# Optimization experiments

Hardware: AMD Instinct MI355X
Metric: run time of the kernel (lower is better)

Reference implementation:

```python
import jax, jax.numpy as jnp
import numpy as np

D_MODEL = 1024
NUM_HEADS = 16
D_K = D_MODEL // NUM_HEADS
ROPE_THETA = 10000.0


def setup_inputs() -> dict:
    key = jax.random.key(0)
    kx, kq, kk, kv, ko = jax.random.split(key, 5)
    B, S = 2, 2048
    sigma = np.sqrt(2.0) / np.sqrt(D_MODEL + D_MODEL)
    x = jax.random.normal(kx, (B, S, D_MODEL), dtype=jnp.float32)
    Wq = jax.random.normal(kq, (D_MODEL, D_MODEL), dtype=jnp.float32) * sigma
    Wk = jax.random.normal(kk, (D_MODEL, D_MODEL), dtype=jnp.float32) * sigma
    Wv = jax.random.normal(kv, (D_MODEL, D_MODEL), dtype=jnp.float32) * sigma
    Wo = jax.random.normal(ko, (D_MODEL, D_MODEL), dtype=jnp.float32) * sigma
    return {"x": x, "Wq": Wq, "Wk": Wk, "Wv": Wv, "Wo": Wo}


def _rope(t, positions):
    # t: [B, H, S, D_K], positions: [S]
    half = jnp.arange(0, D_K, 2, dtype=jnp.float32)          # [D_K/2]
    freqs = 1.0 / (ROPE_THETA ** (half / D_K))               # [D_K/2]
    angles = positions[:, None].astype(jnp.float32) * freqs  # [S, D_K/2]
    cos = jnp.cos(angles)
    sin = jnp.sin(angles)
    t_even = t[..., 0::2]
    t_odd = t[..., 1::2]
    even_rot = t_even * cos - t_odd * sin
    odd_rot = t_even * sin + t_odd * cos
    # interleave back to [..., D_K]
    return jnp.stack([even_rot, odd_rot], axis=-1).reshape(t.shape)


def reference(x, Wq, Wk, Wv, Wo):
    B, S, _ = x.shape
    # weight layout is [d_out, d_in]: y = x @ W.T
    def proj(W):
        y = jnp.einsum('bsd,ed->bse', x, W)
        return y.reshape(B, S, NUM_HEADS, D_K).transpose(0, 2, 1, 3)  # [B,H,S,Dk]
    Q, K, V = proj(Wq), proj(Wk), proj(Wv)
    positions = jnp.arange(S)
    Q = _rope(Q, positions)
    K = _rope(K, positions)
    scale = 1.0 / jnp.sqrt(jnp.asarray(D_K, dtype=x.dtype))
    scores = jnp.einsum('bhqd,bhkd->bhqk', Q, K) * scale  # [B,H,S,S]
    causal = jnp.tril(jnp.ones((S, S), dtype=bool))
    scores = jnp.where(causal, scores, -jnp.inf)
    probs = jax.nn.softmax(scores, axis=-1)
    out = jnp.einsum('bhqk,bhkd->bhqd', probs, V)          # [B,H,S,Dk]
    out = out.transpose(0, 2, 1, 3).reshape(B, S, D_MODEL)
    return jnp.einsum('bsd,ed->bse', out, Wo)
```

## Files before the change

### kernel.cpp

```cpp
#include <hip/hip_runtime.h>
#include <hip/hip_bf16.h>
#include <math.h>

#define S_LEN   2048
#define BATCH   2
#define DMODEL  1024
#define NHEADS  16
#define DKH     64
#define MROWS   (BATCH * S_LEN)

typedef __attribute__((ext_vector_type(8))) __bf16 bf16x8;
typedef __attribute__((ext_vector_type(4))) float f32x4;
typedef __attribute__((ext_vector_type(8))) unsigned short u16x8;

__device__ __forceinline__ float bfu2f(unsigned short u) {
    union { unsigned int i; float f; } v;
    v.i = ((unsigned int)u) << 16;
    return v.f;
}

__device__ __forceinline__ unsigned short f2bfu(float f) {
    union { __bf16 h; unsigned short u; } v;
    v.h = (__bf16)f;
    return v.u;
}

#define LGKM0() __builtin_amdgcn_s_waitcnt(0xc07f)

#define VMCNT_BAR(n) do {                                        \
    asm volatile("s_waitcnt vmcnt(" #n ")" ::: "memory");        \
    __builtin_amdgcn_s_barrier();                                \
    __builtin_amdgcn_sched_barrier(0);                           \
} while (0)

__device__ __forceinline__ void gload_lds16(const void* g, void* l) {
    __builtin_amdgcn_global_load_lds(
        (const __attribute__((address_space(1))) void*)g,
        (__attribute__((address_space(3))) void*)l, 16, 0, 0);
}

__global__ __launch_bounds__(256) void cvt_all(
    const float* __restrict__ W0, const float* __restrict__ W1, const float* __restrict__ W2,
    const float* __restrict__ X,
    unsigned short* __restrict__ Wb,
    unsigned short* __restrict__ Xb)
{
    const int y = blockIdx.y;
    const float* src;
    unsigned short* dst;
    if (y < 3) {
        src = (y == 0) ? W0 : (y == 1) ? W1 : W2;
        dst = Wb + (size_t)y * (DMODEL * DMODEL);
    } else {
        src = X + (size_t)(y - 3) * (DMODEL * DMODEL);
        dst = Xb + (size_t)(y - 3) * (DMODEL * DMODEL);
    }
    size_t idx = ((size_t)blockIdx.x * 256 + threadIdx.x) * 8;
    float4 a = *(const float4*)(src + idx);
    float4 b = *(const float4*)(src + idx + 4);
    u16x8 h;
    h[0] = f2bfu(a.x); h[1] = f2bfu(a.y); h[2] = f2bfu(a.z); h[3] = f2bfu(a.w);
    h[4] = f2bfu(b.x); h[5] = f2bfu(b.y); h[6] = f2bfu(b.z); h[7] = f2bfu(b.w);
    *(u16x8*)(dst + idx) = h;
}

__global__ __launch_bounds__(256) void cvt_wo(
    const float* __restrict__ W, unsigned short* __restrict__ Wob)
{
    size_t idx = ((size_t)blockIdx.x * 256 + threadIdx.x) * 8;
    float4 a = *(const float4*)(W + idx);
    float4 b = *(const float4*)(W + idx + 4);
    u16x8 h;
    h[0] = f2bfu(a.x); h[1] = f2bfu(a.y); h[2] = f2bfu(a.z); h[3] = f2bfu(a.w);
    h[4] = f2bfu(b.x); h[5] = f2bfu(b.y); h[6] = f2bfu(b.z); h[7] = f2bfu(b.w);
    *(u16x8*)(Wob + idx) = h;
}

__global__ __launch_bounds__(256) void gemm_qkv(
    const unsigned short* __restrict__ Xb,
    const unsigned short* __restrict__ Wb,
    unsigned short* __restrict__ Yq, unsigned short* __restrict__ Yk, unsigned short* __restrict__ Yv)
{
    __shared__ __align__(16) unsigned char pool[49152];
    unsigned short* base = (unsigned short*)pool;

    const int tid  = threadIdx.x;
    const int wave = tid >> 6;
    const int lane = tid & 63;
    const int c    = lane & 15;
    const int quad = lane >> 4;

    const int m0 = blockIdx.y * 128;
    const int n0 = blockIdx.x * 128;
    const int w_idx = n0 >> 10;
    const int e0    = n0 & 1023;
    const unsigned short* Wsrc = Wb + (size_t)w_idx * (DMODEL * DMODEL);

    const int mhalf = (wave & 1) * 64;
    const int nhalf = (wave >> 1) * 64;

    f32x4 acc[4][4];
#pragma unroll
    for (int i = 0; i < 4; i++)
#pragma unroll
        for (int j = 0; j < 4; j++) acc[i][j] = (f32x4){0.f, 0.f, 0.f, 0.f};

    const int srow = wave * 32 + (lane >> 2);
    const int scol = (lane & 3) * 8;
    const unsigned short* Asrc = Xb   + (size_t)(m0 + srow) * DMODEL + scol;
    const unsigned short* Bsrc = Wsrc + (size_t)(e0 + srow) * DMODEL + scol;
    const int doff = srow * 32 + scol;

#define QKV_STAGE(buf, kt) do {                                                    \
    unsigned short* _A = base + (buf) * 8192;                                      \
    unsigned short* _B = _A + 4096;                                                \
    const int _k0 = (kt) * 32;                                                     \
    _Pragma("unroll")                                                              \
    for (int _j = 0; _j < 2; _j++) {                                               \
        gload_lds16(Asrc + (size_t)(_j * 16) * DMODEL + _k0, _A + doff + _j * 512);\
        gload_lds16(Bsrc + (size_t)(_j * 16) * DMODEL + _k0, _B + doff + _j * 512);\
    }                                                                              \
} while (0)

#define QKV_COMPUTE(buf) do {                                                      \
    const unsigned short* _A = base + (buf) * 8192;                                \
    const unsigned short* _B = _A + 4096;                                          \
    bf16x8 af[4], bfr[4];                                                          \
    _Pragma("unroll")                                                              \
    for (int mt = 0; mt < 4; mt++)                                                 \
        af[mt] = *(const bf16x8*)(&_A[(mhalf + mt * 16 + c) * 32 + quad * 8]);     \
    _Pragma("unroll")                                                              \
    for (int nt = 0; nt < 4; nt++)                                                 \
        bfr[nt] = *(const bf16x8*)(&_B[(nhalf + nt * 16 + c) * 32 + quad * 8]);    \
    _Pragma("unroll")                                                              \
    for (int mt = 0; mt < 4; mt++)                                                 \
        _Pragma("unroll")                                                          \
        for (int nt = 0; nt < 4; nt++)                                             \
            acc[mt][nt] = __builtin_amdgcn_mfma_f32_16x16x32_bf16(af[mt], bfr[nt], acc[mt][nt], 0, 0, 0); \
} while (0)

    QKV_STAGE(0, 0);
    QKV_STAGE(1, 1);
    for (int g = 0; g < 10; ++g) {
        const int t = g * 3;
        VMCNT_BAR(4); QKV_STAGE(2, t + 2); QKV_COMPUTE(0);
        VMCNT_BAR(4); QKV_STAGE(0, t + 3); QKV_COMPUTE(1);
        VMCNT_BAR(4); QKV_STAGE(1, t + 4); QKV_COMPUTE(2);
    }
    VMCNT_BAR(4); QKV_COMPUTE(0);
    VMCNT_BAR(0); QKV_COMPUTE(1);

    __syncthreads();

    const int h = (e0 + nhalf) >> 6;
    if (w_idx < 2) {
        unsigned short* Yqk = (w_idx == 0) ? Yq : Yk;
        float* EPf = (float*)pool + wave * 16 * 68;
        const int row = lane >> 2;
        const int cg  = lane & 3;
#pragma unroll
        for (int mt = 0; mt < 4; mt++) {
            LGKM0();
#pragma unroll
            for (int nt = 0; nt < 4; nt++)
#pragma unroll
                for (int r = 0; r < 4; r++)
                    EPf[(quad * 4 + r) * 68 + nt * 16 + c] = acc[mt][nt][r];
            LGKM0();
            float fl[16];
#pragma unroll
            for (int j = 0; j < 4; j++) {
                float4 v = *(const float4*)(&EPf[row * 68 + cg * 16 + j * 4]);
                fl[j * 4 + 0] = v.x; fl[j * 4 + 1] = v.y;
                fl[j * 4 + 2] = v.z; fl[j * 4 + 3] = v.w;
            }
            int m = m0 + mhalf + mt * 16 + row;
            int s = m & (S_LEN - 1);
            int b = m >> 11;
            u16x8 o0, o1;
#pragma unroll
            for (int pi = 0; pi < 8; pi++) {
                int p = cg * 8 + pi;
                float freq  = exp2f(-(float)p * 0.41524101186092034f);
                float angle = (float)s * freq;
                float sn, cs;
                __sincosf(angle, &sn, &cs);
                float ev = fl[2 * pi], ov = fl[2 * pi + 1];
                float re = ev * cs - ov * sn;
                float ro = ev * sn + ov * cs;
                if (pi < 4) { o0[2 * pi] = f2bfu(re); o0[2 * pi + 1] = f2bfu(ro); }
                else        { o1[2 * (pi - 4)] = f2bfu(re); o1[2 * (pi - 4) + 1] = f2bfu(ro); }
            }
            unsigned short* dst = Yqk + (((size_t)(b * NHEADS + h)) * S_LEN + s) * DKH + cg * 16;
            *(u16x8*)(dst)     = o0;
            *(u16x8*)(dst + 8) = o1;
        }
    } else {
        unsigned short* EPb = (unsigned short*)pool + wave * 64 * 72;
        LGKM0();
#pragma unroll
        for (int nt = 0; nt < 4; nt++)
#pragma unroll
            for (int mt = 0; mt < 4; mt++)
#pragma unroll
                for (int r = 0; r < 4; r++)
                    EPb[(nt * 16 + c) * 72 + mt * 16 + quad * 4 + r] = f2bfu(acc[mt][nt][r]);
        LGKM0();
        int mbase = m0 + mhalf;
        int s0 = mbase & (S_LEN - 1);
        int b  = mbase >> 11;
        unsigned short* dst = Yv + (((size_t)(b * NHEADS + h)) * DKH + lane) * S_LEN + s0;
#pragma unroll
        for (int j = 0; j < 8; j++)
            *(u16x8*)(dst + j * 8) = *(const u16x8*)(&EPb[lane * 72 + j * 8]);
    }
#undef QKV_STAGE
#undef QKV_COMPUTE
}

__global__ __launch_bounds__(256) void gemm_wo(
    const unsigned short* __restrict__ X,
    const unsigned short* __restrict__ Wob,
    float* __restrict__ Yf)
{
    __shared__ __align__(16) unsigned char pool[36864];
    unsigned short* base = (unsigned short*)pool;

    const int tid  = threadIdx.x;
    const int wave = tid >> 6;
    const int lane = tid & 63;
    const int c    = lane & 15;
    const int quad = lane >> 4;

    const int m0 = blockIdx.y * 64;
    const int n0 = blockIdx.x * 128;

    const int mhalf = (wave & 1) * 32;
    const int nhalf = (wave >> 1) * 64;

    f32x4 acc[2][4];
#pragma unroll
    for (int i = 0; i < 2; i++)
#pragma unroll
        for (int j = 0; j < 4; j++) acc[i][j] = (f32x4){0.f, 0.f, 0.f, 0.f};

    const int arow = wave * 16 + (lane >> 2);
    const int brow = wave * 32 + (lane >> 2);
    const int scol = (lane & 3) * 8;
    const unsigned short* Asrc = X   + (size_t)(m0 + arow) * DMODEL + scol;
    const unsigned short* Bsrc = Wob + (size_t)(n0 + brow) * DMODEL + scol;
    const int adoff = arow * 32 + scol;
    const int bdoff = brow * 32 + scol;

#define WO_STAGE(buf, kt) do {                                                     \
    unsigned short* _A = base + (buf) * 6144;                                      \
    unsigned short* _B = _A + 2048;                                                \
    const int _k0 = (kt) * 32;                                                     \
    gload_lds16(Asrc + _k0, _A + adoff);                                           \
    _Pragma("unroll")                                                              \
    for (int _j = 0; _j < 2; _j++)                                                 \
        gload_lds16(Bsrc + (size_t)(_j * 16) * DMODEL + _k0, _B + bdoff + _j * 512);\
} while (0)

#define WO_COMPUTE(buf) do {                                                       \
    const unsigned short* _A = base + (buf) * 6144;                                \
    const unsigned short* _B = _A + 2048;                                          \
    bf16x8 af[2], bfr[4];                                                          \
    _Pragma("unroll")                                                              \
    for (int mt = 0; mt < 2; mt++)                                                 \
        af[mt] = *(const bf16x8*)(&_A[(mhalf + mt * 16 + c) * 32 + quad * 8]);     \
    _Pragma("unroll")                                                              \
    for (int nt = 0; nt < 4; nt++)                                                 \
        bfr[nt] = *(const bf16x8*)(&_B[(nhalf + nt * 16 + c) * 32 + quad * 8]);    \
    _Pragma("unroll")                                                              \
    for (int mt = 0; mt < 2; mt++)                                                 \
        _Pragma("unroll")                                                          \
        for (int nt = 0; nt < 4; nt++)                                             \
            acc[mt][nt] = __builtin_amdgcn_mfma_f32_16x16x32_bf16(af[mt], bfr[nt], acc[mt][nt], 0, 0, 0); \
} while (0)

    WO_STAGE(0, 0);
    WO_STAGE(1, 1);
    for (int g = 0; g < 10; ++g) {
        const int t = g * 3;
        VMCNT_BAR(3); WO_STAGE(2, t + 2); WO_COMPUTE(0);
        VMCNT_BAR(3); WO_STAGE(0, t + 3); WO_COMPUTE(1);
        VMCNT_BAR(3); WO_STAGE(1, t + 4); WO_COMPUTE(2);
    }
    VMCNT_BAR(3); WO_COMPUTE(0);
    VMCNT_BAR(0); WO_COMPUTE(1);

    __syncthreads();

    float* EPf = (float*)pool + wave * 16 * 68;
    const int row = lane >> 2;
    const int cg  = lane & 3;
#pragma unroll
    for (int mt = 0; mt < 2; mt++) {
        LGKM0();
#pragma unroll
        for (int nt = 0; nt < 4; nt++)
#pragma unroll
            for (int r = 0; r < 4; r++)
                EPf[(quad * 4 + r) * 68 + nt * 16 + c] = acc[mt][nt][r];
        LGKM0();
        int m = m0 + mhalf + mt * 16 + row;
        float* dst = Yf + (size_t)m * DMODEL + n0 + nhalf + cg * 16;
#pragma unroll
        for (int j = 0; j < 4; j++)
            *(float4*)(dst + j * 4) = *(const float4*)(&EPf[row * 68 + cg * 16 + j * 4]);
    }
#undef WO_STAGE
#undef WO_COMPUTE
}

__global__ __launch_bounds__(256, 4) void attn_mfma(
    const unsigned short* __restrict__ Q,
    const unsigned short* __restrict__ K,
    const unsigned short* __restrict__ Vt,
    unsigned short* __restrict__ A)
{
    __shared__ unsigned short Ks[2][32 * 72];
    __shared__ unsigned short Vs[2][64 * 40];
    __shared__ unsigned short Plds[4][16 * 40];

    const int tid  = threadIdx.x;
    const int wave = tid >> 6;
    const int lane = tid & 63;
    const int c    = lane & 15;
    const int quad = lane >> 4;

    const int bh = blockIdx.x;
    const int b  = bh >> 4;
    const int h  = bh & 15;
    const int qb = (int)(gridDim.y - 1) - (int)blockIdx.y;
    const int q0b = qb * 64;
    const int q0 = q0b + wave * 16;

    const unsigned short* Qb = Q  + (size_t)bh * S_LEN * DKH;
    const unsigned short* Kb = K  + (size_t)bh * S_LEN * DKH;
    const unsigned short* Vb = Vt + (size_t)bh * DKH * S_LEN;

    bf16x8 qf0 = *(const bf16x8*)(Qb + (q0 + c) * DKH + quad * 8);
    bf16x8 qf1 = *(const bf16x8*)(Qb + (q0 + c) * DKH + 32 + quad * 8);

    f32x4 o0 = {0.f,0.f,0.f,0.f}, o1 = o0, o2 = o0, o3 = o0;
    float l[4] = {0.f, 0.f, 0.f, 0.f};

    unsigned short* Pw = &Plds[wave][0];

    const int my_nkb   = (q0 + 16 + 31) >> 5;
    const int nkb_blk  = (q0b + 64 + 31) >> 5;
    const int kb_full  = (q0 >= 31) ? (((q0 - 31) >> 5) + 1) : 0;

    const int krow  = tid >> 3;
    const int kcol8 = (tid & 7) * 8;
    const int vrow  = tid >> 2;
    const int vcol8 = (tid & 3) * 8;

    uint4 gK = *(const uint4*)(Kb + (size_t)krow * DKH + kcol8);
    uint4 gV = *(const uint4*)(Vb + (size_t)vrow * S_LEN + vcol8);
    *(uint4*)(&Ks[0][krow * 72 + kcol8]) = gK;
    *(uint4*)(&Vs[0][vrow * 40 + vcol8]) = gV;

    for (int kb = 0; kb < nkb_blk; kb++) {
        const int k0 = kb * 32;
        const int nb = kb + 1;
        const bool pre = nb < nkb_blk;
        __syncthreads();
        if (pre) {
            gK = *(const uint4*)(Kb + (size_t)(nb * 32 + krow) * DKH + kcol8);
            gV = *(const uint4*)(Vb + (size_t)vrow * S_LEN + nb * 32 + vcol8);
        }
        if (kb < my_nkb) {
            const unsigned short* Kc = &Ks[kb & 1][0];
            const unsigned short* Vc = &Vs[kb & 1][0];
            bf16x8 k00 = *(const bf16x8*)(&Kc[c * 72 + quad * 8]);
            bf16x8 k01 = *(const bf16x8*)(&Kc[c * 72 + 32 + quad * 8]);
            bf16x8 k10 = *(const bf16x8*)(&Kc[(16 + c) * 72 + quad * 8]);
            bf16x8 k11 = *(const bf16x8*)(&Kc[(16 + c) * 72 + 32 + quad * 8]);
            f32x4 s0 = {0.f,0.f,0.f,0.f}, s1 = {0.f,0.f,0.f,0.f};
            __builtin_amdgcn_s_setprio(1);
            s0 = __builtin_amdgcn_mfma_f32_16x16x32_bf16(qf0, k00, s0, 0, 0, 0);
            s0 = __builtin_amdgcn_mfma_f32_16x16x32_bf16(qf1, k01, s0, 0, 0, 0);
            s1 = __builtin_amdgcn_mfma_f32_16x16x32_bf16(qf0, k10, s1, 0, 0, 0);
            s1 = __builtin_amdgcn_mfma_f32_16x16x32_bf16(qf1, k11, s1, 0, 0, 0);
            __builtin_amdgcn_s_setprio(0);

            if (kb < kb_full) {
#pragma unroll
                for (int r = 0; r < 4; r++) {
                    float e0 = __expf(s0[r] * 0.125f);
                    float e1 = __expf(s1[r] * 0.125f);
                    unsigned short pb0 = f2bfu(e0);
                    unsigned short pb1 = f2bfu(e1);
                    Pw[(quad * 4 + r) * 40 + c]      = pb0;
                    Pw[(quad * 4 + r) * 40 + 16 + c] = pb1;
                    l[r] += bfu2f(pb0) + bfu2f(pb1);
                }
            } else {
#pragma unroll
                for (int r = 0; r < 4; r++) {
                    int qrow = q0 + quad * 4 + r;
                    float e0 = (k0 + c      <= qrow) ? __expf(s0[r] * 0.125f) : 0.0f;
                    float e1 = (k0 + 16 + c <= qrow) ? __expf(s1[r] * 0.125f) : 0.0f;
                    unsigned short pb0 = f2bfu(e0);
                    unsigned short pb1 = f2bfu(e1);
                    Pw[(quad * 4 + r) * 40 + c]      = pb0;
                    Pw[(quad * 4 + r) * 40 + 16 + c] = pb1;
                    l[r] += bfu2f(pb0) + bfu2f(pb1);
                }
            }
            LGKM0();

            bf16x8 pf = *(const bf16x8*)(Pw + c * 40 + quad * 8);

            bf16x8 vf0 = *(const bf16x8*)(&Vc[(0 * 16 + c) * 40 + quad * 8]);
            bf16x8 vf1 = *(const bf16x8*)(&Vc[(1 * 16 + c) * 40 + quad * 8]);
            bf16x8 vf2 = *(const bf16x8*)(&Vc[(2 * 16 + c) * 40 + quad * 8]);
            bf16x8 vf3 = *(const bf16x8*)(&Vc[(3 * 16 + c) * 40 + quad * 8]);
            __builtin_amdgcn_s_setprio(1);
            o0 = __builtin_amdgcn_mfma_f32_16x16x32_bf16(pf, vf0, o0, 0, 0, 0);
            o1 = __builtin_amdgcn_mfma_f32_16x16x32_bf16(pf, vf1, o1, 0, 0, 0);
            o2 = __builtin_amdgcn_mfma_f32_16x16x32_bf16(pf, vf2, o2, 0, 0, 0);
            o3 = __builtin_amdgcn_mfma_f32_16x16x32_bf16(pf, vf3, o3, 0, 0, 0);
            __builtin_amdgcn_s_setprio(0);
        }
        if (pre) {
            *(uint4*)(&Ks[nb & 1][krow * 72 + kcol8]) = gK;
            *(uint4*)(&Vs[nb & 1][vrow * 40 + vcol8]) = gV;
        }
    }

#pragma unroll
    for (int m = 1; m < 16; m <<= 1) {
#pragma unroll
        for (int r = 0; r < 4; r++) l[r] += __shfl_xor(l[r], m, 64);
    }

#pragma unroll
    for (int r = 0; r < 4; r++) {
        float inv = 1.0f / l[r];
        int s = q0 + quad * 4 + r;
        unsigned short* Ap = A + ((size_t)b * S_LEN + s) * DMODEL + h * DKH;
        Ap[0 * 16 + c] = f2bfu(o0[r] * inv);
        Ap[1 * 16 + c] = f2bfu(o1[r] * inv);
        Ap[2 * 16 + c] = f2bfu(o2[r] * inv);
        Ap[3 * 16 + c] = f2bfu(o3[r] * inv);
    }
}

extern "C" void kernel_launch(void* const* d_in, const int* in_sizes, int n_in,
                              void* d_out, int out_size, void* d_ws, size_t ws_size,
                              hipStream_t stream) {
    const float* x  = (const float*)d_in[0];
    const float* Wq = (const float*)d_in[1];
    const float* Wk = (const float*)d_in[2];
    const float* Wv = (const float*)d_in[3];
    const float* Wo = (const float*)d_in[4];
    float* out = (float*)d_out;

    unsigned short* Qw = (unsigned short*)d_ws;
    unsigned short* Kw = Qw + (size_t)MROWS * DMODEL;
    unsigned short* Vw = Kw + (size_t)MROWS * DMODEL;
    unsigned short* Wb = Vw + (size_t)MROWS * DMODEL;
    unsigned short* Aw = Wb;
    unsigned short* Wob = Qw;
    unsigned short* Xb = (unsigned short*)d_out;

    cvt_all<<<dim3(DMODEL * DMODEL / (256 * 8), 7), 256, 0, stream>>>(Wq, Wk, Wv, x, Wb, Xb);

    gemm_qkv<<<dim3(3 * DMODEL / 128, MROWS / 128), 256, 0, stream>>>(
        Xb, Wb, Qw, Kw, Vw);

    attn_mfma<<<dim3(NHEADS * BATCH, S_LEN / 64), 256, 0, stream>>>(Qw, Kw, Vw, Aw);

    cvt_wo<<<dim3(DMODEL * DMODEL / (256 * 8)), 256, 0, stream>>>(Wo, Wob);

    gemm_wo<<<dim3(DMODEL / 128, MROWS / 64), 256, 0, stream>>>(Aw, Wob, out);
}
```

Before: 190.7 us.

## Shrink attention blocks to two waves with 32-query tiles

The attention kernel now uses 128-thread blocks covering 32 query rows instead of 256-thread blocks covering 64, which doubles the grid along the query axis. Each thread loads twice as much K/V data per tile, and because both waves now share the same key-block count, the per-wave causal guard goes away. The aim is finer-grained causal load balancing and less idle time for waves on the diagonal. In exchange, every K/V tile is loaded from global memory by twice as many blocks, and each block has fewer waves to hide latency behind its barriers.

```diff
diff --git a/kernel.cpp b/kernel.cpp
--- a/kernel.cpp
+++ b/kernel.cpp
@@ -314,7 +314,7 @@
 #undef WO_COMPUTE
 }
 
-__global__ __launch_bounds__(256, 4) void attn_mfma(
+__global__ __launch_bounds__(128, 4) void attn_mfma(
     const unsigned short* __restrict__ Q,
     const unsigned short* __restrict__ K,
     const unsigned short* __restrict__ Vt,
@@ -322,7 +322,7 @@
 {
     __shared__ unsigned short Ks[2][32 * 72];
     __shared__ unsigned short Vs[2][64 * 40];
-    __shared__ unsigned short Plds[4][16 * 40];
+    __shared__ unsigned short Plds[2][16 * 40];
 
     const int tid  = threadIdx.x;
     const int wave = tid >> 6;
@@ -334,8 +334,8 @@
     const int b  = bh >> 4;
     const int h  = bh & 15;
     const int qb = (int)(gridDim.y - 1) - (int)blockIdx.y;
-    const int q0b = qb * 64;
-    const int q0 = q0b + wave * 16;
+    const int q0b = qb * 32;
+    const int q0  = q0b + wave * 16;
 
     const unsigned short* Qb = Q  + (size_t)bh * S_LEN * DKH;
     const unsigned short* Kb = K  + (size_t)bh * S_LEN * DKH;
@@ -349,30 +349,35 @@
 
     unsigned short* Pw = &Plds[wave][0];
 
-    const int my_nkb   = (q0 + 16 + 31) >> 5;
-    const int nkb_blk  = (q0b + 64 + 31) >> 5;
-    const int kb_full  = (q0 >= 31) ? (((q0 - 31) >> 5) + 1) : 0;
-
-    const int krow  = tid >> 3;
-    const int kcol8 = (tid & 7) * 8;
-    const int vrow  = tid >> 2;
-    const int vcol8 = (tid & 3) * 8;
-
-    uint4 gK = *(const uint4*)(Kb + (size_t)krow * DKH + kcol8);
-    uint4 gV = *(const uint4*)(Vb + (size_t)vrow * S_LEN + vcol8);
-    *(uint4*)(&Ks[0][krow * 72 + kcol8]) = gK;
-    *(uint4*)(&Vs[0][vrow * 40 + vcol8]) = gV;
-
-    for (int kb = 0; kb < nkb_blk; kb++) {
+    const int nkb     = qb + 1;
+    const int kb_full = (q0 >= 31) ? (((q0 - 31) >> 5) + 1) : 0;
+
+    const int krow = tid >> 2;
+    const int kcol = (tid & 3) * 16;
+    const int vrow = tid >> 1;
+    const int vcol = (tid & 1) * 16;
+
+    uint4 gK0 = *(const uint4*)(Kb + (size_t)krow * DKH + kcol);
+    uint4 gK1 = *(const uint4*)(Kb + (size_t)krow * DKH + kcol + 8);
+    uint4 gV0 = *(const uint4*)(Vb + (size_t)vrow * S_LEN + vcol);
+    uint4 gV1 = *(const uint4*)(Vb + (size_t)vrow * S_LEN + vcol + 8);
+    *(uint4*)(&Ks[0][krow * 72 + kcol])     = gK0;
+    *(uint4*)(&Ks[0][krow * 72 + kcol + 8]) = gK1;
+    *(uint4*)(&Vs[0][vrow * 40 + vcol])     = gV0;
+    *(uint4*)(&Vs[0][vrow * 40 + vcol + 8]) = gV1;
+
+    for (int kb = 0; kb < nkb; kb++) {
         const int k0 = kb * 32;
         const int nb = kb + 1;
-        const bool pre = nb < nkb_blk;
+        const bool pre = nb < nkb;
         __syncthreads();
         if (pre) {
-            gK = *(const uint4*)(Kb + (size_t)(nb * 32 + krow) * DKH + kcol8);
-            gV = *(const uint4*)(Vb + (size_t)vrow * S_LEN + nb * 32 + vcol8);
+            gK0 = *(const uint4*)(Kb + (size_t)(nb * 32 + krow) * DKH + kcol);
+            gK1 = *(const uint4*)(Kb + (size_t)(nb * 32 + krow) * DKH + kcol + 8);
+            gV0 = *(const uint4*)(Vb + (size_t)vrow * S_LEN + nb * 32 + vcol);
+            gV1 = *(const uint4*)(Vb + (size_t)vrow * S_LEN + nb * 32 + vcol + 8);
         }
-        if (kb < my_nkb) {
+        {
             const unsigned short* Kc = &Ks[kb & 1][0];
             const unsigned short* Vc = &Vs[kb & 1][0];
             bf16x8 k00 = *(const bf16x8*)(&Kc[c * 72 + quad * 8]);
@@ -427,8 +432,10 @@
             __builtin_amdgcn_s_setprio(0);
         }
         if (pre) {
-            *(uint4*)(&Ks[nb & 1][krow * 72 + kcol8]) = gK;
-            *(uint4*)(&Vs[nb & 1][vrow * 40 + vcol8]) = gV;
+            *(uint4*)(&Ks[nb & 1][krow * 72 + kcol])     = gK0;
+            *(uint4*)(&Ks[nb & 1][krow * 72 + kcol + 8]) = gK1;
+            *(uint4*)(&Vs[nb & 1][vrow * 40 + vcol])     = gV0;
+            *(uint4*)(&Vs[nb & 1][vrow * 40 + vcol + 8]) = gV1;
         }
     }
 
@@ -473,7 +480,7 @@
     gemm_qkv<<<dim3(3 * DMODEL / 128, MROWS / 128), 256, 0, stream>>>(
         Xb, Wb, Qw, Kw, Vw);
 
-    attn_mfma<<<dim3(NHEADS * BATCH, S_LEN / 64), 256, 0, stream>>>(Qw, Kw, Vw, Aw);
+    attn_mfma<<<dim3(NHEADS * BATCH, S_LEN / 32), 128, 0, stream>>>(Qw, Kw, Vw, Aw);
 
     cvt_wo<<<dim3(DMODEL * DMODEL / (256 * 8)), 256, 0, stream>>>(Wo, Wob);
 
```

Result: no change. 192.6 us (+1.0%).

## Split long causal query blocks across two KV halves and add combine kernel

Applied to the files above, without the earlier changes.

Query blocks 17-31 (the longest causal rows) now have their KV range split into two halves, each processed by a separate workgroup. Partial unnormalized outputs and row sums go to a scratch buffer in the output memory, and a new combine kernel merges them. Short blocks are still handled by a single workgroup. This balances per-block work so the longest blocks no longer set the tail of the attention kernel. The cost is an extra launch and extra scratch traffic. Launch bounds also rise to 8 waves per SIMD. The merge only sums outputs and sums without a max rescale, which relies on the kernel not tracking a running max.

```diff
diff --git a/kernel.cpp b/kernel.cpp
--- a/kernel.cpp
+++ b/kernel.cpp
@@ -8,6 +8,11 @@
 #define NHEADS  16
 #define DKH     64
 #define MROWS   (BATCH * S_LEN)
+
+#define SPLIT_Q0   17
+#define NPIECE     47
+#define SLOTS_BH   30
+#define PO_FLOATS  (960 * 4096)
 
 typedef __attribute__((ext_vector_type(8))) __bf16 bf16x8;
 typedef __attribute__((ext_vector_type(4))) float f32x4;
@@ -314,11 +319,12 @@
 #undef WO_COMPUTE
 }
 
-__global__ __launch_bounds__(256, 4) void attn_mfma(
+__global__ __launch_bounds__(256, 8) void attn_mfma(
     const unsigned short* __restrict__ Q,
     const unsigned short* __restrict__ K,
     const unsigned short* __restrict__ Vt,
-    unsigned short* __restrict__ A)
+    unsigned short* __restrict__ A,
+    float* __restrict__ Scr)
 {
     __shared__ unsigned short Ks[2][32 * 72];
     __shared__ unsigned short Vs[2][64 * 40];
@@ -333,9 +339,23 @@
     const int bh = blockIdx.x;
     const int b  = bh >> 4;
     const int h  = bh & 15;
-    const int qb = (int)(gridDim.y - 1) - (int)blockIdx.y;
+
+    const int R = (int)blockIdx.y;
+    int qb, t_lo, t_hi, spl = 0;
+    bool is_split;
+    if (R <= 16) {
+        qb = 16 - R; t_lo = 0; t_hi = 2 * qb + 2; is_split = false;
+    } else {
+        int i = R - 17;
+        qb  = 31 - (i >> 1);
+        spl = i & 1;
+        int nk = 2 * qb + 2, half = nk >> 1;
+        t_lo = spl ? half : 0;
+        t_hi = spl ? nk   : half;
+        is_split = true;
+    }
     const int q0b = qb * 64;
-    const int q0 = q0b + wave * 16;
+    const int q0  = q0b + wave * 16;
 
     const unsigned short* Qb = Q  + (size_t)bh * S_LEN * DKH;
     const unsigned short* Kb = K  + (size_t)bh * S_LEN * DKH;
@@ -350,7 +370,6 @@
     unsigned short* Pw = &Plds[wave][0];
 
     const int my_nkb   = (q0 + 16 + 31) >> 5;
-    const int nkb_blk  = (q0b + 64 + 31) >> 5;
     const int kb_full  = (q0 >= 31) ? (((q0 - 31) >> 5) + 1) : 0;
 
     const int krow  = tid >> 3;
@@ -358,15 +377,15 @@
     const int vrow  = tid >> 2;
     const int vcol8 = (tid & 3) * 8;
 
-    uint4 gK = *(const uint4*)(Kb + (size_t)krow * DKH + kcol8);
-    uint4 gV = *(const uint4*)(Vb + (size_t)vrow * S_LEN + vcol8);
-    *(uint4*)(&Ks[0][krow * 72 + kcol8]) = gK;
-    *(uint4*)(&Vs[0][vrow * 40 + vcol8]) = gV;
-
-    for (int kb = 0; kb < nkb_blk; kb++) {
+    uint4 gK = *(const uint4*)(Kb + (size_t)(t_lo * 32 + krow) * DKH + kcol8);
+    uint4 gV = *(const uint4*)(Vb + (size_t)vrow * S_LEN + t_lo * 32 + vcol8);
+    *(uint4*)(&Ks[t_lo & 1][krow * 72 + kcol8]) = gK;
+    *(uint4*)(&Vs[t_lo & 1][vrow * 40 + vcol8]) = gV;
+
+    for (int kb = t_lo; kb < t_hi; kb++) {
         const int k0 = kb * 32;
         const int nb = kb + 1;
-        const bool pre = nb < nkb_blk;
+        const bool pre = nb < t_hi;
         __syncthreads();
         if (pre) {
             gK = *(const uint4*)(Kb + (size_t)(nb * 32 + krow) * DKH + kcol8);
@@ -438,16 +457,74 @@
         for (int r = 0; r < 4; r++) l[r] += __shfl_xor(l[r], m, 64);
     }
 
-#pragma unroll
-    for (int r = 0; r < 4; r++) {
-        float inv = 1.0f / l[r];
-        int s = q0 + quad * 4 + r;
-        unsigned short* Ap = A + ((size_t)b * S_LEN + s) * DMODEL + h * DKH;
-        Ap[0 * 16 + c] = f2bfu(o0[r] * inv);
-        Ap[1 * 16 + c] = f2bfu(o1[r] * inv);
-        Ap[2 * 16 + c] = f2bfu(o2[r] * inv);
-        Ap[3 * 16 + c] = f2bfu(o3[r] * inv);
-    }
+    if (!is_split) {
+#pragma unroll
+        for (int r = 0; r < 4; r++) {
+            float inv = 1.0f / l[r];
+            int s = q0 + quad * 4 + r;
+            unsigned short* Ap = A + ((size_t)b * S_LEN + s) * DMODEL + h * DKH;
+            Ap[0 * 16 + c] = f2bfu(o0[r] * inv);
+            Ap[1 * 16 + c] = f2bfu(o1[r] * inv);
+            Ap[2 * 16 + c] = f2bfu(o2[r] * inv);
+            Ap[3 * 16 + c] = f2bfu(o3[r] * inv);
+        }
+    } else {
+        const int slot = bh * SLOTS_BH + (qb - SPLIT_Q0) * 2 + spl;
+        float* Po = Scr + (size_t)slot * 4096;
+        float* Pl = Scr + PO_FLOATS + (size_t)slot * 64;
+#pragma unroll
+        for (int r = 0; r < 4; r++) {
+            int row = wave * 16 + quad * 4 + r;
+            Po[row * 64 + 0 * 16 + c] = o0[r];
+            Po[row * 64 + 1 * 16 + c] = o1[r];
+            Po[row * 64 + 2 * 16 + c] = o2[r];
+            Po[row * 64 + 3 * 16 + c] = o3[r];
+            if (c == 0) Pl[row] = l[r];
+        }
+    }
+}
+
+__global__ __launch_bounds__(256) void attn_combine(
+    const float* __restrict__ Scr, unsigned short* __restrict__ A)
+{
+    const int bx  = blockIdx.x;
+    const int bh  = bx / 15;
+    const int qbm = bx % 15;
+    const int qb  = SPLIT_Q0 + qbm;
+    const int b   = bh >> 4;
+    const int h   = bh & 15;
+
+    const int slot0 = bh * SLOTS_BH + qbm * 2;
+    const float* O0 = Scr + (size_t)slot0 * 4096;
+    const float* O1 = O0 + 4096;
+    const float* L0 = Scr + PO_FLOATS + (size_t)slot0 * 64;
+    const float* L1 = L0 + 64;
+
+    const int r  = threadIdx.x >> 2;
+    const int cg = (threadIdx.x & 3) * 16;
+
+    float inv = 1.0f / (L0[r] + L1[r]);
+
+    u16x8 outv[2];
+#pragma unroll
+    for (int half = 0; half < 2; half++) {
+        float4 a0 = *(const float4*)(O0 + r * 64 + cg + half * 8);
+        float4 b0 = *(const float4*)(O0 + r * 64 + cg + half * 8 + 4);
+        float4 a1 = *(const float4*)(O1 + r * 64 + cg + half * 8);
+        float4 b1 = *(const float4*)(O1 + r * 64 + cg + half * 8 + 4);
+        outv[half][0] = f2bfu((a0.x + a1.x) * inv);
+        outv[half][1] = f2bfu((a0.y + a1.y) * inv);
+        outv[half][2] = f2bfu((a0.z + a1.z) * inv);
+        outv[half][3] = f2bfu((a0.w + a1.w) * inv);
+        outv[half][4] = f2bfu((b0.x + b1.x) * inv);
+        outv[half][5] = f2bfu((b0.y + b1.y) * inv);
+        outv[half][6] = f2bfu((b0.z + b1.z) * inv);
+        outv[half][7] = f2bfu((b0.w + b1.w) * inv);
+    }
+    const int s = qb * 64 + r;
+    unsigned short* Ap = A + ((size_t)b * S_LEN + s) * DMODEL + h * DKH + cg;
+    *(u16x8*)(Ap)     = outv[0];
+    *(u16x8*)(Ap + 8) = outv[1];
 }
 
 extern "C" void kernel_launch(void* const* d_in, const int* in_sizes, int n_in,
@@ -467,13 +544,16 @@
     unsigned short* Aw = Wb;
     unsigned short* Wob = Qw;
     unsigned short* Xb = (unsigned short*)d_out;
+    float* Scr = (float*)d_out;
 
     cvt_all<<<dim3(DMODEL * DMODEL / (256 * 8), 7), 256, 0, stream>>>(Wq, Wk, Wv, x, Wb, Xb);
 
     gemm_qkv<<<dim3(3 * DMODEL / 128, MROWS / 128), 256, 0, stream>>>(
         Xb, Wb, Qw, Kw, Vw);
 
-    attn_mfma<<<dim3(NHEADS * BATCH, S_LEN / 64), 256, 0, stream>>>(Qw, Kw, Vw, Aw);
+    attn_mfma<<<dim3(NHEADS * BATCH, NPIECE), 256, 0, stream>>>(Qw, Kw, Vw, Aw, Scr);
+
+    attn_combine<<<dim3(NHEADS * BATCH * 15), 256, 0, stream>>>(Scr, Aw);
 
     cvt_wo<<<dim3(DMODEL * DMODEL / (256 * 8)), 256, 0, stream>>>(Wo, Wob);
 
```

After: 189.7 us. About the same (-0.5%).
